# Kernel optimization log

Hardware: AMD Instinct MI355X
Metric: run time of the kernel (lower is better)

The kernel has to match this reference:

```python
import jax, jax.numpy as jnp
import numpy as np

NUM_FEATURES = 5
MUL_FACTOR = 2.0


def setup_inputs() -> dict:
    key = jax.random.key(0)
    x = jax.random.normal(key, (4096, 512), dtype=jnp.float32)
    # buffer from __init__: mul_factor ** (arange(F) - F // 2)
    bandwidth_multipliers = (MUL_FACTOR ** (jnp.arange(NUM_FEATURES) - NUM_FEATURES // 2)).astype(jnp.float32)
    return {"x": x, "bandwidth_multipliers": bandwidth_multipliers}


def _cdist(x):
    # pairwise Euclidean distance, p=2
    sq = jnp.sum(x * x, axis=1)
    d2 = sq[:, None] + sq[None, :] - 2.0 * (x @ x.T)
    return jnp.sqrt(jnp.maximum(d2, 0.0))


def reference(x, bandwidth_multipliers):
    d = _cdist(x)  # [N, N]
    n = d.shape[0]
    # heuristic bandwidth on detached distances (self.bandwidth is None)
    bw = jax.lax.stop_gradient(d).sum() / (n * (n - 1))
    bws = bw * bandwidth_multipliers  # [F]
    # exp over F bandwidths, summed: [F, N, N] -> [N, N]
    return jnp.exp(-d[None, :, :] / bws[:, None, None]).sum(axis=0)
```

## Files before the change

### kernel.cpp

```cpp
#include <hip/hip_runtime.h>
#include <cstdint>
#include <cstddef>

#define N_PTS 4096
#define KDIM  512
#define NFEAT 5

typedef __attribute__((ext_vector_type(8))) short bf16x8;
typedef __attribute__((ext_vector_type(4))) float f32x4;
typedef uint32_t u32;

__device__ inline unsigned short f2bf(float f) {
  union { float f; u32 u; } v; v.f = f;
  u32 r = (v.u + 0x7fffu + ((v.u >> 16) & 1u)) >> 16;
  return (unsigned short)r;
}

__device__ inline void load_lds16(const void* g, void* l) {
  __builtin_amdgcn_global_load_lds(
      (const __attribute__((address_space(1))) void*)g,
      (__attribute__((address_space(3))) void*)l, 16, 0, 0);
}

__global__ __launch_bounds__(256) void prep_kernel(const float* __restrict__ X,
                                                   short* __restrict__ Xb,
                                                   float* __restrict__ sq,
                                                   float* __restrict__ gsum) {
  if (blockIdx.x == 0 && threadIdx.x == 0) *gsum = 0.f;
  const int row = blockIdx.x;
  const int t = threadIdx.x;
  const float2 v = ((const float2*)(X + (size_t)row * KDIM))[t];
  short2 b;
  b.x = (short)f2bf(v.x);
  b.y = (short)f2bf(v.y);
  ((short2*)(Xb + (size_t)row * KDIM))[t] = b;
  float s = v.x * v.x + v.y * v.y;
#pragma unroll
  for (int off = 32; off; off >>= 1) s += __shfl_down(s, off);
  __shared__ float ws[4];
  if ((t & 63) == 0) ws[t >> 6] = s;
  __syncthreads();
  if (t == 0) sq[row] = ws[0] + ws[1] + ws[2] + ws[3];
}

#define GEMM_TILE(bm, bn, acc, As, Bs)                                        \
  {                                                                           \
    const size_t ga0 = (size_t)((bm)*128 + srow) * KDIM + sgran * 8;          \
    const size_t gb0 = (size_t)((bn)*128 + srow) * KDIM + sgran * 8;          \
    for (int kt = 0; kt < KDIM / 64; ++kt) {                                  \
      const int koff = kt * 64;                                               \
      _Pragma("unroll") for (int g = 0; g < 4; ++g) {                         \
        load_lds16(Xb + ga0 + (size_t)g * 32 * KDIM + koff,                   \
                   (char*)As + g * 4096 + tid * 16);                          \
        load_lds16(Xb + gb0 + (size_t)g * 32 * KDIM + koff,                   \
                   (char*)Bs + g * 4096 + tid * 16);                          \
      }                                                                       \
      __syncthreads();                                                        \
      _Pragma("unroll") for (int h = 0; h < 2; ++h) {                         \
        bf16x8 a[4], b[4];                                                    \
        _Pragma("unroll") for (int i = 0; i < 4; ++i) {                       \
          const int ra = wave_m * 64 + i * 16 + llo;                          \
          const int rb = wave_n * 64 + i * 16 + llo;                          \
          const int c = h * 4 + lhi;                                          \
          a[i] = *(const bf16x8*)&As[ra * 64 + ((c ^ (ra & 7)) << 3)];        \
          b[i] = *(const bf16x8*)&Bs[rb * 64 + ((c ^ (rb & 7)) << 3)];        \
        }                                                                     \
        _Pragma("unroll") for (int i = 0; i < 4; ++i)                         \
            _Pragma("unroll") for (int j = 0; j < 4; ++j)                     \
                acc[i][j] = __builtin_amdgcn_mfma_f32_16x16x32_bf16(          \
                    a[i], b[j], acc[i][j], 0, 0, 0);                          \
      }                                                                       \
      __syncthreads();                                                        \
    }                                                                         \
  }

__global__ __launch_bounds__(256, 2) void sum_kernel(
    const short* __restrict__ Xb, const float* __restrict__ sq,
    float* __restrict__ gsum) {
  __shared__ short As[128 * 64];
  __shared__ short Bs[128 * 64];
  __shared__ float red[4];

  const int tid = threadIdx.x;
  const int lane = tid & 63;
  const int wid = tid >> 6;
  const int wave_m = wid >> 1, wave_n = wid & 1;
  const int lhi = lane >> 4, llo = lane & 15;
  const int srow = tid >> 3;
  const int sgran = (tid & 7) ^ (srow & 7);

  int t = (int)blockIdx.x;
  int bm = 0;
  while (t >= 32 - bm) { t -= 32 - bm; ++bm; }
  const int bn = bm + t;

  f32x4 acc[4][4];
#pragma unroll
  for (int i = 0; i < 4; ++i)
#pragma unroll
    for (int j = 0; j < 4; ++j) acc[i][j] = (f32x4){0.f, 0.f, 0.f, 0.f};

  GEMM_TILE(bm, bn, acc, As, Bs);

  float lsum = 0.f;
  const int gi0 = bm * 128, gj0 = bn * 128;
  const int r_base = wave_m * 64 + lhi * 4;
  const int c_base = wave_n * 64 + llo;
  float sqj[4];
#pragma unroll
  for (int j = 0; j < 4; ++j) sqj[j] = sq[gj0 + c_base + j * 16];
#pragma unroll
  for (int i = 0; i < 4; ++i) {
#pragma unroll
    for (int rr = 0; rr < 4; ++rr) {
      const int r = r_base + i * 16 + rr;
      const float sqi = sq[gi0 + r];
#pragma unroll
      for (int j = 0; j < 4; ++j) {
        const int c = c_base + j * 16;
        const float d2 = sqi + sqj[j] - 2.f * acc[i][j][rr];
        float dd = sqrtf(fmaxf(d2, 0.f));
        if (gi0 + r == gj0 + c) dd = 0.f;
        lsum += dd;
      }
    }
  }

#pragma unroll
  for (int off = 32; off; off >>= 1) lsum += __shfl_down(lsum, off);
  if (lane == 0) red[wid] = lsum;
  __syncthreads();
  if (tid == 0) {
    const float w = (bm == bn) ? 1.f : 2.f;
    atomicAdd(gsum, w * (red[0] + red[1] + red[2] + red[3]));
  }
}

__global__ __launch_bounds__(256, 2) void rbf_kernel(
    const short* __restrict__ Xb, const float* __restrict__ sq,
    const float* __restrict__ mult, const float* __restrict__ gsum,
    float* __restrict__ out) {
  __shared__ short As[128 * 64];
  __shared__ short Bs[128 * 64];

  const int tid = threadIdx.x;
  const int lane = tid & 63;
  const int wid = tid >> 6;
  const int wave_m = wid >> 1, wave_n = wid & 1;
  const int lhi = lane >> 4, llo = lane & 15;
  const int srow = tid >> 3;
  const int sgran = (tid & 7) ^ (srow & 7);

  const int bm = blockIdx.y, bn = blockIdx.x;

  const float bw = *gsum * (1.0f / ((float)N_PTS * (float)(N_PTS - 1)));
  float cf[NFEAT];
#pragma unroll
  for (int f = 0; f < NFEAT; ++f) cf[f] = -1.0f / (bw * mult[f]);

  f32x4 acc[4][4];
#pragma unroll
  for (int i = 0; i < 4; ++i)
#pragma unroll
    for (int j = 0; j < 4; ++j) acc[i][j] = (f32x4){0.f, 0.f, 0.f, 0.f};

  GEMM_TILE(bm, bn, acc, As, Bs);

  const int gi0 = bm * 128, gj0 = bn * 128;
  const int r_base = wave_m * 64 + lhi * 4;
  const int c_base = wave_n * 64 + llo;
  float sqj[4];
#pragma unroll
  for (int j = 0; j < 4; ++j) sqj[j] = sq[gj0 + c_base + j * 16];
#pragma unroll
  for (int i = 0; i < 4; ++i) {
#pragma unroll
    for (int rr = 0; rr < 4; ++rr) {
      const int r = r_base + i * 16 + rr;
      const float sqi = sq[gi0 + r];
      float* orow = out + (size_t)(gi0 + r) * N_PTS + gj0;
#pragma unroll
      for (int j = 0; j < 4; ++j) {
        const int c = c_base + j * 16;
        float d2 = sqi + sqj[j] - 2.f * acc[i][j][rr];
        float dd = sqrtf(fmaxf(d2, 0.f));
        if (gi0 + r == gj0 + c) dd = 0.f;
        float a = 0.f;
#pragma unroll
        for (int f = 0; f < NFEAT; ++f) a += __expf(dd * cf[f]);
        orow[c] = a;
      }
    }
  }
}

extern "C" void kernel_launch(void* const* d_in, const int* in_sizes, int n_in,
                              void* d_out, int out_size, void* d_ws, size_t ws_size,
                              hipStream_t stream) {
  const float* X = (const float*)d_in[0];
  const float* mult = (const float*)d_in[1];
  float* out = (float*)d_out;

  char* ws = (char*)d_ws;
  float* gsum = (float*)ws;
  float* sq = (float*)(ws + 1024);
  short* Xb = (short*)(ws + 1024 + N_PTS * sizeof(float));

  prep_kernel<<<N_PTS, 256, 0, stream>>>(X, Xb, sq, gsum);
  sum_kernel<<<528, 256, 0, stream>>>(Xb, sq, gsum);
  rbf_kernel<<<dim3(32, 32), 256, 0, stream>>>(Xb, sq, mult, gsum, out);
}
```

Before: 131.0 us.

## Cache bf16 distances, exploit symmetry, and derive RBF sums from one exp

The distance kernel now stores each upper-triangle tile's distances as bf16 in workspace. The RBF kernel reads them instead of recomputing the GEMM, and it writes both the tile and its transpose through LDS. When the multipliers equal powers of two, the five exponentials come from one exp via squaring and square roots. This removes the second GEMM and half the exp work, at the cost of extra workspace traffic and bf16 rounding of distances.

```diff
diff --git a/kernel.cpp b/kernel.cpp
--- a/kernel.cpp
+++ b/kernel.cpp
@@ -5,6 +5,7 @@
 #define N_PTS 4096
 #define KDIM  512
 #define NFEAT 5
+#define NTILES 528
 
 typedef __attribute__((ext_vector_type(8))) short bf16x8;
 typedef __attribute__((ext_vector_type(4))) float f32x4;
@@ -14,6 +15,12 @@
   union { float f; u32 u; } v; v.f = f;
   u32 r = (v.u + 0x7fffu + ((v.u >> 16) & 1u)) >> 16;
   return (unsigned short)r;
+}
+
+__device__ inline void bf2f2(u32 u, float& a, float& b) {
+  union { u32 u; float f; } x, y;
+  x.u = u << 16; y.u = u & 0xffff0000u;
+  a = x.f; b = y.f;
 }
 
 __device__ inline void load_lds16(const void* g, void* l) {
@@ -74,9 +81,9 @@
     }                                                                         \
   }
 
-__global__ __launch_bounds__(256, 2) void sum_kernel(
+__global__ __launch_bounds__(256, 2) void dist_kernel(
     const short* __restrict__ Xb, const float* __restrict__ sq,
-    float* __restrict__ gsum) {
+    unsigned short* __restrict__ Dw, float* __restrict__ gsum) {
   __shared__ short As[128 * 64];
   __shared__ short Bs[128 * 64];
   __shared__ float red[4];
@@ -109,8 +116,13 @@
   float sqj[4];
 #pragma unroll
   for (int j = 0; j < 4; ++j) sqj[j] = sq[gj0 + c_base + j * 16];
+
+  const size_t tile_base =
+      (size_t)blockIdx.x * 16384 + (size_t)wid * 4096;
+
 #pragma unroll
   for (int i = 0; i < 4; ++i) {
+    union { unsigned short s[16]; uint4 q[2]; } pk;
 #pragma unroll
     for (int rr = 0; rr < 4; ++rr) {
       const int r = r_base + i * 16 + rr;
@@ -118,12 +130,16 @@
 #pragma unroll
       for (int j = 0; j < 4; ++j) {
         const int c = c_base + j * 16;
-        const float d2 = sqi + sqj[j] - 2.f * acc[i][j][rr];
+        float d2 = sqi + sqj[j] - 2.f * acc[i][j][rr];
         float dd = sqrtf(fmaxf(d2, 0.f));
         if (gi0 + r == gj0 + c) dd = 0.f;
         lsum += dd;
+        pk.s[rr * 4 + j] = f2bf(dd);
       }
     }
+    unsigned short* dst = Dw + tile_base + (size_t)i * 1024;
+    *(uint4*)(dst + lane * 8) = pk.q[0];
+    *(uint4*)(dst + 512 + lane * 8) = pk.q[1];
   }
 
 #pragma unroll
@@ -136,60 +152,104 @@
   }
 }
 
-__global__ __launch_bounds__(256, 2) void rbf_kernel(
-    const short* __restrict__ Xb, const float* __restrict__ sq,
-    const float* __restrict__ mult, const float* __restrict__ gsum,
-    float* __restrict__ out) {
-  __shared__ short As[128 * 64];
-  __shared__ short Bs[128 * 64];
+__global__ __launch_bounds__(256) void rbf_kernel(
+    const unsigned short* __restrict__ Dw, const float* __restrict__ gsum,
+    const float* __restrict__ mult, float* __restrict__ out) {
+  __shared__ float T[32 * 132];
 
   const int tid = threadIdx.x;
   const int lane = tid & 63;
   const int wid = tid >> 6;
   const int wave_m = wid >> 1, wave_n = wid & 1;
   const int lhi = lane >> 4, llo = lane & 15;
-  const int srow = tid >> 3;
-  const int sgran = (tid & 7) ^ (srow & 7);
-
-  const int bm = blockIdx.y, bn = blockIdx.x;
+
+  int t = (int)blockIdx.x;
+  int bm = 0;
+  while (t >= 32 - bm) { t -= 32 - bm; ++bm; }
+  const int bn = bm + t;
+  const bool diag = (bm == bn);
 
   const float bw = *gsum * (1.0f / ((float)N_PTS * (float)(N_PTS - 1)));
+  const float m0 = mult[0], m1 = mult[1], m2 = mult[2], m3 = mult[3],
+              m4 = mult[4];
+  const bool fast = (m0 == 0.25f && m1 == 0.5f && m2 == 1.0f && m3 == 2.0f &&
+                     m4 == 4.0f);
+  const float c1 = -1.0f / (bw * m2);
   float cf[NFEAT];
-#pragma unroll
-  for (int f = 0; f < NFEAT; ++f) cf[f] = -1.0f / (bw * mult[f]);
-
-  f32x4 acc[4][4];
-#pragma unroll
-  for (int i = 0; i < 4; ++i)
-#pragma unroll
-    for (int j = 0; j < 4; ++j) acc[i][j] = (f32x4){0.f, 0.f, 0.f, 0.f};
-
-  GEMM_TILE(bm, bn, acc, As, Bs);
+  cf[0] = -1.0f / (bw * m0); cf[1] = -1.0f / (bw * m1); cf[2] = c1;
+  cf[3] = -1.0f / (bw * m3); cf[4] = -1.0f / (bw * m4);
+
+  const size_t tile_base =
+      (size_t)blockIdx.x * 16384 + (size_t)wid * 4096;
+
+  uint4 q[4][2];
+#pragma unroll
+  for (int i = 0; i < 4; ++i) {
+    const unsigned short* src = Dw + tile_base + (size_t)i * 1024;
+    q[i][0] = *(const uint4*)(src + lane * 8);
+    q[i][1] = *(const uint4*)(src + 512 + lane * 8);
+  }
 
   const int gi0 = bm * 128, gj0 = bn * 128;
-  const int r_base = wave_m * 64 + lhi * 4;
-  const int c_base = wave_n * 64 + llo;
-  float sqj[4];
-#pragma unroll
-  for (int j = 0; j < 4; ++j) sqj[j] = sq[gj0 + c_base + j * 16];
+  const int r_off = wave_m * 64 + lhi * 4;
+  const int c_off = wave_n * 64 + llo;
+
 #pragma unroll
   for (int i = 0; i < 4; ++i) {
+    float v[16];
+    bf2f2(q[i][0].x, v[0], v[1]);   bf2f2(q[i][0].y, v[2], v[3]);
+    bf2f2(q[i][0].z, v[4], v[5]);   bf2f2(q[i][0].w, v[6], v[7]);
+    bf2f2(q[i][1].x, v[8], v[9]);   bf2f2(q[i][1].y, v[10], v[11]);
+    bf2f2(q[i][1].z, v[12], v[13]); bf2f2(q[i][1].w, v[14], v[15]);
+
+    float o[16];
+    if (fast) {
+#pragma unroll
+      for (int e = 0; e < 16; ++e) {
+        const float tt = __expf(v[e] * c1);
+        const float t2 = tt * tt;
+        const float t4 = t2 * t2;
+        const float s = sqrtf(tt);
+        const float qq = sqrtf(s);
+        o[e] = t4 + t2 + tt + s + qq;
+      }
+    } else {
+#pragma unroll
+      for (int e = 0; e < 16; ++e) {
+        float a = 0.f;
+#pragma unroll
+        for (int f = 0; f < NFEAT; ++f) a += __expf(v[e] * cf[f]);
+        o[e] = a;
+      }
+    }
+
 #pragma unroll
     for (int rr = 0; rr < 4; ++rr) {
-      const int r = r_base + i * 16 + rr;
-      const float sqi = sq[gi0 + r];
-      float* orow = out + (size_t)(gi0 + r) * N_PTS + gj0;
-#pragma unroll
-      for (int j = 0; j < 4; ++j) {
-        const int c = c_base + j * 16;
-        float d2 = sqi + sqj[j] - 2.f * acc[i][j][rr];
-        float dd = sqrtf(fmaxf(d2, 0.f));
-        if (gi0 + r == gj0 + c) dd = 0.f;
-        float a = 0.f;
-#pragma unroll
-        for (int f = 0; f < NFEAT; ++f) a += __expf(dd * cf[f]);
-        orow[c] = a;
-      }
+      float* orow = out + (size_t)(gi0 + r_off + i * 16 + rr) * N_PTS + gj0;
+#pragma unroll
+      for (int j = 0; j < 4; ++j) orow[c_off + j * 16] = o[rr * 4 + j];
+    }
+
+    if (!diag) {
+#pragma unroll
+      for (int rr = 0; rr < 4; ++rr)
+#pragma unroll
+        for (int j = 0; j < 4; ++j)
+          T[(wave_m * 16 + lhi * 4 + rr) * 132 + wave_n * 64 + j * 16 + llo] =
+              o[rr * 4 + j];
+      __syncthreads();
+      const int c = tid >> 1;
+      const int g = tid & 1;
+      float w[16];
+#pragma unroll
+      for (int k = 0; k < 16; ++k) w[k] = T[(g * 16 + k) * 132 + c];
+      float* mrow =
+          out + (size_t)(gj0 + c) * N_PTS + gi0 + g * 64 + i * 16;
+      *(float4*)(mrow + 0) = (float4){w[0], w[1], w[2], w[3]};
+      *(float4*)(mrow + 4) = (float4){w[4], w[5], w[6], w[7]};
+      *(float4*)(mrow + 8) = (float4){w[8], w[9], w[10], w[11]};
+      *(float4*)(mrow + 12) = (float4){w[12], w[13], w[14], w[15]};
+      __syncthreads();
     }
   }
 }
@@ -205,8 +265,10 @@
   float* gsum = (float*)ws;
   float* sq = (float*)(ws + 1024);
   short* Xb = (short*)(ws + 1024 + N_PTS * sizeof(float));
+  unsigned short* Dw = (unsigned short*)(ws + 1024 + N_PTS * sizeof(float) +
+                                         (size_t)N_PTS * KDIM * sizeof(short));
 
   prep_kernel<<<N_PTS, 256, 0, stream>>>(X, Xb, sq, gsum);
-  sum_kernel<<<528, 256, 0, stream>>>(Xb, sq, gsum);
-  rbf_kernel<<<dim3(32, 32), 256, 0, stream>>>(Xb, sq, mult, gsum, out);
-}
+  dist_kernel<<<NTILES, 256, 0, stream>>>(Xb, sq, Dw, gsum);
+  rbf_kernel<<<NTILES, 256, 0, stream>>>(Dw, gsum, mult, out);
+}
```

New measurement: 122.3 us, median of 2. 6.7% less time.
